# Optimization experiments

Hardware: AMD Instinct MI355X
Metric: run time of the kernel (lower is better)

The kernel has to match this reference:

```python
import jax, jax.numpy as jnp
import numpy as np

D_MODEL, D_INNER, D_STATE, D_CONV, DT_RANK = 512, 1024, 64, 4, 32
B, L = 2, 1000
EPS = 1e-5


def _rmsnorm(x, w):
    return x * jax.lax.rsqrt(jnp.mean(x * x, axis=-1, keepdims=True) + EPS) * w


def _causal_dwconv(x, w, b):
    # x: (B, L, Di); w: (Di, K) depthwise causal conv, output length L
    xT = jnp.transpose(x, (0, 2, 1))  # (B, Di, L)
    y = jax.lax.conv_general_dilated(
        xT, w[:, None, :], window_strides=(1,), padding=[(D_CONV - 1, 0)],
        dimension_numbers=('NCH', 'OIH', 'NCH'), feature_group_count=D_INNER)
    return jnp.transpose(y + b[None, :, None], (0, 2, 1))


def _selective_scan(u, dt, A, Bm, Cm):
    # u, dt: (B, L, Di); A: (Di, N); Bm, Cm: (B, L, N)
    def step(h, inp):
        dt_t, B_t, C_t, u_t = inp
        dA = jnp.exp(dt_t[..., None] * A)                       # (B, Di, N)
        h = dA * h + (dt_t * u_t)[..., None] * B_t[:, None, :]  # state update
        y = jnp.einsum('bdn,bn->bd', h, C_t)
        return h, y
    xs = (jnp.swapaxes(dt, 0, 1), jnp.swapaxes(Bm, 0, 1),
          jnp.swapaxes(Cm, 0, 1), jnp.swapaxes(u, 0, 1))
    h0 = jnp.zeros((u.shape[0], D_INNER, D_STATE), u.dtype)
    _, ys = jax.lax.scan(step, h0, xs)
    return jnp.swapaxes(ys, 0, 1)  # (B, L, Di)


def _mamba_layer(x, norm_w, in_proj, conv_w, conv_b, x_proj, dt_w, dt_b, A_log, Dp, out_proj):
    # mamba-ssm Block with fused_add_norm=False, n_layer=1:
    # residual = x; h = mixer(rmsnorm(x)); block output pair merges to h + x
    h = _rmsnorm(x, norm_w)
    xz = jnp.einsum('bld,ed->ble', h, in_proj)        # (B, L, 2*Di)
    xc, z = jnp.split(xz, 2, axis=-1)
    xc = jax.nn.silu(_causal_dwconv(xc, conv_w, conv_b))
    x_dbl = jnp.einsum('bld,ed->ble', xc, x_proj)     # (B, L, dt_rank + 2N)
    dt, Bm, Cm = jnp.split(x_dbl, [DT_RANK, DT_RANK + D_STATE], axis=-1)
    dt = jax.nn.softplus(jnp.einsum('blr,dr->bld', dt, dt_w) + dt_b)
    A = -jnp.exp(A_log)
    y = _selective_scan(xc, dt, A, Bm, Cm)
    y = (y + xc * Dp) * jax.nn.silu(z)
    return jnp.einsum('bld,ed->ble', y, out_proj) + x


def _forward(x,
             f_norm_w, f_in_proj, f_conv_w, f_conv_b, f_x_proj, f_dt_w, f_dt_b, f_A_log, f_D, f_out_proj,
             b_norm_w, b_in_proj, b_conv_w, b_conv_b, b_x_proj, b_dt_w, b_dt_b, b_A_log, b_D, b_out_proj):
    res_f = _mamba_layer(x, f_norm_w, f_in_proj, f_conv_w, f_conv_b, f_x_proj,
                         f_dt_w, f_dt_b, f_A_log, f_D, f_out_proj)
    res_b = _mamba_layer(jnp.flip(x, 1), b_norm_w, b_in_proj, b_conv_w, b_conv_b,
                         b_x_proj, b_dt_w, b_dt_b, b_A_log, b_D, b_out_proj)
    return res_f + jnp.flip(res_b, 1)  # bidirectional_merging='add'


def setup_inputs() -> dict:
    key = jax.random.key(0)
    ks = iter(jax.random.split(key, 32))
    def nrm(shape, s=0.02):
        return jax.random.normal(next(ks), shape, jnp.float32) * s
    inp = {'x': jax.random.normal(next(ks), (B, L, D_MODEL), jnp.float32)}
    for p in ('f', 'b'):
        inp[p + '_norm_w'] = jnp.ones((D_MODEL,), jnp.float32)
        inp[p + '_in_proj'] = nrm((2 * D_INNER, D_MODEL))
        inp[p + '_conv_w'] = nrm((D_INNER, D_CONV), 0.1)
        inp[p + '_conv_b'] = nrm((D_INNER,), 0.1)
        inp[p + '_x_proj'] = nrm((DT_RANK + 2 * D_STATE, D_INNER))
        inp[p + '_dt_w'] = nrm((D_INNER, DT_RANK), 0.1)
        inp[p + '_dt_b'] = jnp.full((D_INNER,), float(np.log(np.expm1(0.01))), jnp.float32)
        inp[p + '_A_log'] = jnp.log(jnp.tile(jnp.arange(1, D_STATE + 1, dtype=jnp.float32), (D_INNER, 1)))
        inp[p + '_D'] = jnp.ones((D_INNER,), jnp.float32)
        inp[p + '_out_proj'] = nrm((D_MODEL, D_INNER))
    return inp


def reference(x,
              f_norm_w, f_in_proj, f_conv_w, f_conv_b, f_x_proj, f_dt_w, f_dt_b, f_A_log, f_D, f_out_proj,
              b_norm_w, b_in_proj, b_conv_w, b_conv_b, b_x_proj, b_dt_w, b_dt_b, b_A_log, b_D, b_out_proj):
    return _forward(x,
                    f_norm_w, f_in_proj, f_conv_w, f_conv_b, f_x_proj, f_dt_w, f_dt_b, f_A_log, f_D, f_out_proj,
                    b_norm_w, b_in_proj, b_conv_w, b_conv_b, b_x_proj, b_dt_w, b_dt_b, b_A_log, b_D, b_out_proj)
```

## Files before the change

### kernel.cpp

```cpp
#include <hip/hip_runtime.h>
#include <hip/hip_bf16.h>
#include <math.h>

#define DM   512
#define DI   1024
#define NS   64
#define RDT  32
#define BB   2
#define LL   1000
#define MROWS (BB*LL)

typedef __attribute__((ext_vector_type(8))) short bf16x8;
typedef __attribute__((ext_vector_type(4))) float f32x4;

__device__ __forceinline__ unsigned short f2bf(float f) {
    unsigned u = __builtin_bit_cast(unsigned, f);
    u = (u + 0x7FFF + ((u >> 16) & 1)) >> 16;
    return (unsigned short)u;
}

__device__ __forceinline__ float bcast_lane(float v, int lane) {
    return __builtin_bit_cast(float,
        __builtin_amdgcn_readlane(__builtin_bit_cast(int, v), lane));
}

__global__ __launch_bounds__(256)
void rmsnorm_k(const float* __restrict__ x,
               const float* __restrict__ nw0, const float* __restrict__ nw1,
               unsigned short* __restrict__ xnb0, unsigned short* __restrict__ xnb1) {
    int row = blockIdx.x;
    int tid = threadIdx.x;
    const float* xr = x + (size_t)row * DM;
    float2 v = *(const float2*)(xr + tid * 2);
    float ss = v.x * v.x + v.y * v.y;
    #pragma unroll
    for (int off = 32; off; off >>= 1) ss += __shfl_xor(ss, off, 64);
    __shared__ float red[4];
    if ((tid & 63) == 0) red[tid >> 6] = ss;
    __syncthreads();
    float tot = red[0] + red[1] + red[2] + red[3];
    float scale = rsqrtf(tot / (float)DM + 1e-5f);
    float2 w0 = *(const float2*)(nw0 + tid * 2);
    float2 w1 = *(const float2*)(nw1 + tid * 2);
    short2 o0, o1;
    o0.x = (short)f2bf(v.x * scale * w0.x);
    o0.y = (short)f2bf(v.y * scale * w0.y);
    o1.x = (short)f2bf(v.x * scale * w1.x);
    o1.y = (short)f2bf(v.y * scale * w1.y);
    *(short2*)(xnb0 + (size_t)row * DM + tid * 2) = o0;
    *(short2*)(xnb1 + (size_t)row * DM + tid * 2) = o1;
}

__global__ __launch_bounds__(256)
void cvt2_k(const float* __restrict__ in0, const float* __restrict__ in1,
            unsigned short* __restrict__ out0, unsigned short* __restrict__ out1,
            int n4) {
    int idx = blockIdx.x * 256 + threadIdx.x;
    if (idx >= n4) return;
    const float* in = blockIdx.y ? in1 : in0;
    unsigned short* out = blockIdx.y ? out1 : out0;
    float4 v = *(const float4*)(in + (size_t)idx * 4);
    short4 o;
    o.x = (short)f2bf(v.x); o.y = (short)f2bf(v.y);
    o.z = (short)f2bf(v.z); o.w = (short)f2bf(v.w);
    *(short4*)(out + (size_t)idx * 4) = o;
}

__global__ __launch_bounds__(256, 2)
void gemm1_mfma(const unsigned short* __restrict__ xnb0,
                const unsigned short* __restrict__ xnb1,
                const unsigned short* __restrict__ wib0,
                const unsigned short* __restrict__ wib1,
                float* __restrict__ xz0, float* __restrict__ xz1)
{
    __shared__ __align__(16) unsigned short As[128 * 40];
    __shared__ __align__(16) unsigned short Bs[128 * 40];
    int dir = blockIdx.z;
    const unsigned short* A = dir ? xnb1 : xnb0;
    const unsigned short* W = dir ? wib1 : wib0;
    float* C = dir ? xz1 : xz0;
    int n0 = blockIdx.x * 128, m0 = blockIdx.y * 128;
    int tid = threadIdx.x;
    int wv = tid >> 6, lane = tid & 63;
    int wr = wv >> 1, wc = wv & 1;
    int fl = lane & 15, kg = lane >> 4;

    f32x4 acc[4][4];
    #pragma unroll
    for (int i = 0; i < 4; i++)
        #pragma unroll
        for (int j = 0; j < 4; j++) acc[i][j] = (f32x4){0.f, 0.f, 0.f, 0.f};

    int sr = tid >> 2, cg = tid & 3;
    for (int k0 = 0; k0 < 512; k0 += 32) {
        #pragma unroll
        for (int i = 0; i < 2; i++) {
            int row = sr + i * 64;
            int m = m0 + row;
            float4 av = make_float4(0.f, 0.f, 0.f, 0.f);
            if (m < MROWS) {
                int rs = m;
                if (dir) { int b = m / LL, t = m % LL; rs = b * LL + (LL - 1 - t); }
                av = *(const float4*)(A + (size_t)rs * 512 + k0 + cg * 8);
            }
            *(float4*)(&As[row * 40 + cg * 8]) = av;
            float4 wv4 = *(const float4*)(W + (size_t)(n0 + row) * 512 + k0 + cg * 8);
            *(float4*)(&Bs[row * 40 + cg * 8]) = wv4;
        }
        __syncthreads();
        bf16x8 af[4], bf[4];
        #pragma unroll
        for (int fr = 0; fr < 4; fr++)
            af[fr] = *(const bf16x8*)(&As[(wr * 64 + fr * 16 + fl) * 40 + kg * 8]);
        #pragma unroll
        for (int fc = 0; fc < 4; fc++)
            bf[fc] = *(const bf16x8*)(&Bs[(wc * 64 + fc * 16 + fl) * 40 + kg * 8]);
        #pragma unroll
        for (int fr = 0; fr < 4; fr++)
            #pragma unroll
            for (int fc = 0; fc < 4; fc++)
                acc[fr][fc] = __builtin_amdgcn_mfma_f32_16x16x32_bf16(
                    af[fr], bf[fc], acc[fr][fc], 0, 0, 0);
        __syncthreads();
    }
    #pragma unroll
    for (int fr = 0; fr < 4; fr++)
        #pragma unroll
        for (int fc = 0; fc < 4; fc++)
            #pragma unroll
            for (int j = 0; j < 4; j++) {
                int m = m0 + wr * 64 + fr * 16 + kg * 4 + j;
                if (m < MROWS) {
                    int n = n0 + wc * 64 + fc * 16 + fl;
                    C[(size_t)m * 2048 + n] = acc[fr][fc][j];
                }
            }
}

__global__ __launch_bounds__(256, 2)
void gemm_out_mfma(const unsigned short* __restrict__ ygb0,
                   const unsigned short* __restrict__ ygb1,
                   const unsigned short* __restrict__ wob0,
                   const unsigned short* __restrict__ wob1,
                   float* __restrict__ partial)
{
    __shared__ __align__(16) unsigned short As[64 * 40];
    __shared__ __align__(16) unsigned short Bs[64 * 40];
    int dir = blockIdx.z;
    const unsigned short* A = dir ? ygb1 : ygb0;
    const unsigned short* W = dir ? wob1 : wob0;
    float* P = partial + (size_t)dir * MROWS * 512;
    int n0 = blockIdx.x * 64, m0 = blockIdx.y * 64;
    int tid = threadIdx.x;
    int wv = tid >> 6, lane = tid & 63;
    int wr = wv >> 1, wc = wv & 1;
    int fl = lane & 15, kg = lane >> 4;

    f32x4 acc[2][2];
    #pragma unroll
    for (int i = 0; i < 2; i++)
        #pragma unroll
        for (int j = 0; j < 2; j++) acc[i][j] = (f32x4){0.f, 0.f, 0.f, 0.f};

    int sr = tid >> 2, cg = tid & 3;
    for (int k0 = 0; k0 < 1024; k0 += 32) {
        int m = m0 + sr;
        float4 av = make_float4(0.f, 0.f, 0.f, 0.f);
        if (m < MROWS)
            av = *(const float4*)(A + (size_t)m * 1024 + k0 + cg * 8);
        *(float4*)(&As[sr * 40 + cg * 8]) = av;
        float4 wv4 = *(const float4*)(W + (size_t)(n0 + sr) * 1024 + k0 + cg * 8);
        *(float4*)(&Bs[sr * 40 + cg * 8]) = wv4;
        __syncthreads();
        bf16x8 af[2], bf[2];
        #pragma unroll
        for (int fr = 0; fr < 2; fr++)
            af[fr] = *(const bf16x8*)(&As[(wr * 32 + fr * 16 + fl) * 40 + kg * 8]);
        #pragma unroll
        for (int fc = 0; fc < 2; fc++)
            bf[fc] = *(const bf16x8*)(&Bs[(wc * 32 + fc * 16 + fl) * 40 + kg * 8]);
        #pragma unroll
        for (int fr = 0; fr < 2; fr++)
            #pragma unroll
            for (int fc = 0; fc < 2; fc++)
                acc[fr][fc] = __builtin_amdgcn_mfma_f32_16x16x32_bf16(
                    af[fr], bf[fc], acc[fr][fc], 0, 0, 0);
        __syncthreads();
    }
    #pragma unroll
    for (int fr = 0; fr < 2; fr++)
        #pragma unroll
        for (int fc = 0; fc < 2; fc++)
            #pragma unroll
            for (int j = 0; j < 4; j++) {
                int m = m0 + wr * 32 + fr * 16 + kg * 4 + j;
                if (m < MROWS) {
                    int n = n0 + wc * 32 + fc * 16 + fl;
                    P[(size_t)m * 512 + n] = acc[fr][fc][j];
                }
            }
}

__global__ __launch_bounds__(256)
void reduce_out_k(const float* __restrict__ x, const float* __restrict__ partial,
                  float* __restrict__ out)
{
    int idx = blockIdx.x * 256 + threadIdx.x;
    if (idx >= MROWS * 128) return;
    int m = idx >> 7, q = idx & 127;
    int b = m / LL, t = m % LL;
    int fm = b * LL + (LL - 1 - t);
    const float* p0 = partial;
    const float* p1 = partial + (size_t)MROWS * 512;
    float4 xv = *(const float4*)(x  + (size_t)m  * 512 + q * 4);
    float4 a  = *(const float4*)(p0 + (size_t)m  * 512 + q * 4);
    float4 c  = *(const float4*)(p1 + (size_t)fm * 512 + q * 4);
    float4 o;
    o.x = 2.f * xv.x + a.x + c.x;
    o.y = 2.f * xv.y + a.y + c.y;
    o.z = 2.f * xv.z + a.z + c.z;
    o.w = 2.f * xv.w + a.w + c.w;
    *(float4*)(out + (size_t)m * 512 + q * 4) = o;
}

__global__ __launch_bounds__(256)
void conv_silu_k(const float* __restrict__ xz0, const float* __restrict__ xz1,
                 const float* __restrict__ cw0, const float* __restrict__ cw1,
                 const float* __restrict__ cb0, const float* __restrict__ cb1,
                 float* __restrict__ xcT0, float* __restrict__ xcT1)
{
    __shared__ float Ls[64 * 65];
    int dirb = blockIdx.z;
    int dir = dirb >> 1, b = dirb & 1;
    int d0 = blockIdx.x * 64, t0 = blockIdx.y * 64;
    int tid = threadIdx.x;
    int dl = tid & 63, tg = tid >> 6;

    const float* in = (dir ? xz1 : xz0) + (size_t)b * LL * 2048;
    const float* cw = dir ? cw1 : cw0;
    const float* cb = dir ? cb1 : cb0;
    float*      xcT = dir ? xcT1 : xcT0;

    float4 w4 = ((const float4*)cw)[d0 + dl];
    float bias = cb[d0 + dl];

    int ts = t0 + tg * 16;
    float x3 = 0.f, x2 = 0.f, x1 = 0.f;
    if (ts - 3 >= 0 && ts - 3 < LL) x3 = in[(size_t)(ts - 3) * 2048 + d0 + dl];
    if (ts - 2 >= 0 && ts - 2 < LL) x2 = in[(size_t)(ts - 2) * 2048 + d0 + dl];
    if (ts - 1 >= 0 && ts - 1 < LL) x1 = in[(size_t)(ts - 1) * 2048 + d0 + dl];

    #pragma unroll
    for (int i = 0; i < 16; i++) {
        int t = ts + i;
        float x0v = (t < LL) ? in[(size_t)t * 2048 + d0 + dl] : 0.f;
        float a = bias + x3 * w4.x + x2 * w4.y + x1 * w4.z + x0v * w4.w;
        float s = a / (1.f + __expf(-a));
        Ls[dl * 65 + tg * 16 + i] = s;
        x3 = x2; x2 = x1; x1 = x0v;
    }
    __syncthreads();
    int tl = tid & 63, dg = tid >> 6;
    #pragma unroll
    for (int i = 0; i < 16; i++) {
        int dd = dg * 16 + i;
        int t = t0 + tl;
        if (t < LL)
            xcT[((size_t)(b * 1024) + d0 + dd) * LL + t] = Ls[dd * 65 + tl];
    }
}

__global__ __launch_bounds__(256)
void gemm_xp_k(const float* __restrict__ xcT0, const float* __restrict__ xcT1,
               const float* __restrict__ xp0, const float* __restrict__ xp1,
               float* __restrict__ xd0, float* __restrict__ xd1,
               float* __restrict__ bct)
{
    __shared__ float As[16 * 68];
    __shared__ float Ws[16 * 68];
    __shared__ float T[64 * 67];
    int dirb = blockIdx.z;
    int dir = dirb >> 1, b = dirb & 1;
    const float* xcT = (dir ? xcT1 : xcT0) + (size_t)b * 1024 * LL;
    const float* W   = dir ? xp1 : xp0;
    float*       C   = (dir ? xd1 : xd0) + (size_t)b * LL * 160;
    int n0 = blockIdx.x * 64, t0 = blockIdx.y * 64;
    int tid = threadIdx.x;
    int tx = tid & 15, ty = tid >> 4;

    float acc[4][4] = {};

    for (int k0 = 0; k0 < 1024; k0 += 16) {
        {
            int kk = tid & 15, mq = tid >> 4;
            float4 v = make_float4(0.f, 0.f, 0.f, 0.f);
            if (t0 + mq * 4 + 3 < LL)
                v = *(const float4*)(xcT + (size_t)(k0 + kk) * LL + t0 + mq * 4);
            *(float4*)(As + kk * 68 + mq * 4) = v;
        }
        {
            int row = tid >> 2, q = tid & 3;
            float4 v = make_float4(0.f, 0.f, 0.f, 0.f);
            if (n0 + row < 160)
                v = *(const float4*)(W + (size_t)(n0 + row) * 1024 + k0 + q * 4);
            Ws[(q * 4 + 0) * 68 + row] = v.x;
            Ws[(q * 4 + 1) * 68 + row] = v.y;
            Ws[(q * 4 + 2) * 68 + row] = v.z;
            Ws[(q * 4 + 3) * 68 + row] = v.w;
        }
        __syncthreads();
        #pragma unroll
        for (int k = 0; k < 16; k++) {
            float4 a = *(const float4*)(As + k * 68 + ty * 4);
            float4 w = *(const float4*)(Ws + k * 68 + tx * 4);
            float av[4] = {a.x, a.y, a.z, a.w};
            float wvv[4] = {w.x, w.y, w.z, w.w};
            #pragma unroll
            for (int i = 0; i < 4; i++)
                #pragma unroll
                for (int j = 0; j < 4; j++)
                    acc[i][j] = fmaf(av[i], wvv[j], acc[i][j]);
        }
        __syncthreads();
    }

    if (n0 == 0) {
        #pragma unroll
        for (int i = 0; i < 4; i++) {
            int t = t0 + ty * 4 + i;
            if (t >= LL) continue;
            #pragma unroll
            for (int j = 0; j < 4; j++) {
                int n = tx * 4 + j;
                C[(size_t)t * 160 + n] = acc[i][j];
            }
        }
    }

    #pragma unroll
    for (int i = 0; i < 4; i++)
        #pragma unroll
        for (int j = 0; j < 4; j++)
            T[(tx * 4 + j) * 67 + ty * 4 + i] = acc[i][j];
    __syncthreads();
    int tl = tid & 63, ng = tid >> 6;
    #pragma unroll
    for (int i = 0; i < 16; i++) {
        int nl = ng * 16 + i;
        int n = n0 + nl;
        int t = t0 + tl;
        if (n >= 32 && n < 160 && t < LL)
            bct[((size_t)dirb * 128 + (n - 32)) * LL + t] = T[nl * 67 + tl];
    }
}

__global__ __launch_bounds__(256)
void gemm_dt_k(const float* __restrict__ xd0, const float* __restrict__ xd1,
               const float* __restrict__ w0, const float* __restrict__ w1,
               const float* __restrict__ bb0, const float* __restrict__ bb1,
               float* __restrict__ dtT0, float* __restrict__ dtT1)
{
    __shared__ float As[64 * 33];
    __shared__ float Ws[32 * 68];
    __shared__ float T[64 * 67];
    int dirb = blockIdx.z;
    int dir = dirb >> 1, b = dirb & 1;
    const float* xd = (dir ? xd1 : xd0) + (size_t)b * LL * 160;
    const float* W  = dir ? w1 : w0;
    const float* bi = dir ? bb1 : bb0;
    float*      dtT = (dir ? dtT1 : dtT0) + (size_t)b * 1024 * LL;
    int n0 = blockIdx.x * 64, t0 = blockIdx.y * 64;
    int tid = threadIdx.x;
    int tx = tid & 15, ty = tid >> 4;

    #pragma unroll
    for (int i = 0; i < 2; i++) {
        int j = tid + 256 * i;
        int row = j >> 3, q = j & 7;
        float4 v = make_float4(0.f, 0.f, 0.f, 0.f);
        if (t0 + row < LL)
            v = *(const float4*)(xd + (size_t)(t0 + row) * 160 + q * 4);
        As[row * 33 + q * 4 + 0] = v.x;
        As[row * 33 + q * 4 + 1] = v.y;
        As[row * 33 + q * 4 + 2] = v.z;
        As[row * 33 + q * 4 + 3] = v.w;
        float4 wv = *(const float4*)(W + (size_t)(n0 + row) * 32 + q * 4);
        Ws[(q * 4 + 0) * 68 + row] = wv.x;
        Ws[(q * 4 + 1) * 68 + row] = wv.y;
        Ws[(q * 4 + 2) * 68 + row] = wv.z;
        Ws[(q * 4 + 3) * 68 + row] = wv.w;
    }
    __syncthreads();

    float acc[4][4] = {};
    #pragma unroll 8
    for (int k = 0; k < 32; k++) {
        float4 w = *(const float4*)(Ws + k * 68 + tx * 4);
        float wvv[4] = {w.x, w.y, w.z, w.w};
        float av[4];
        #pragma unroll
        for (int i = 0; i < 4; i++) av[i] = As[(ty * 4 + i) * 33 + k];
        #pragma unroll
        for (int i = 0; i < 4; i++)
            #pragma unroll
            for (int j = 0; j < 4; j++)
                acc[i][j] = fmaf(av[i], wvv[j], acc[i][j]);
    }
    __syncthreads();

    #pragma unroll
    for (int i = 0; i < 4; i++) {
        #pragma unroll
        for (int j = 0; j < 4; j++) {
            int n = tx * 4 + j;
            float v = acc[i][j] + bi[n0 + n];
            v = (v > 20.f) ? v : log1pf(__expf(v));
            T[n * 67 + ty * 4 + i] = v;
        }
    }
    __syncthreads();

    int tl = tid & 63, ng = tid >> 6;
    #pragma unroll
    for (int i = 0; i < 16; i++) {
        int nl = ng * 16 + i;
        int t = t0 + tl;
        if (t < LL)
            dtT[(size_t)(n0 + nl) * LL + t] = T[nl * 67 + tl];
    }
}

__global__ __launch_bounds__(256)
void scan_k(float* __restrict__ dtT0, float* __restrict__ dtT1,
            const float* __restrict__ ucT0, const float* __restrict__ ucT1,
            const float* __restrict__ bct,
            const float* __restrict__ Al0, const float* __restrict__ Al1,
            const float* __restrict__ Dc0, const float* __restrict__ Dc1)
{
    __shared__ float Bs[64 * 34];
    __shared__ float Cs[64 * 34];
    __shared__ float Pt[4][16 * 66];
    int dirb = blockIdx.y;
    int dir = dirb >> 1, b = dirb & 1;
    int wid = threadIdx.x >> 6, lane = threadIdx.x & 63;
    int d = blockIdx.x * 4 + wid;
    float* Pw = Pt[wid];

    float*       dtT = (dir ? dtT1 : dtT0);
    const float* ucT = (dir ? ucT1 : ucT0);
    const float* Al  = dir ? Al1 : Al0;
    const float* Dc  = dir ? Dc1 : Dc0;

    float a    = -__expf(Al[d * 64 + lane]) * 1.44269504f;
    float Dp64 = Dc[d] * (1.f / 64.f);
    float h    = 0.f;
    size_t chan = ((size_t)(b * 1024 + d)) * LL;
    const float* Bg = bct + (size_t)dirb * 128 * LL;

    int srow = threadIdx.x >> 2;
    int scol = (threadIdx.x & 3) * 8;
    int tl16 = lane & 15, qq = lane >> 4;
    const float* Prow = Pw + tl16 * 66 + qq * 16;

    for (int t0 = 0; t0 < LL; t0 += 32) {
        int rem = min(32, LL - t0);
        __syncthreads();
        {
            float4 b0 = *(const float4*)(Bg + (size_t)srow * LL + t0 + scol);
            float4 b1 = *(const float4*)(Bg + (size_t)srow * LL + t0 + scol + 4);
            float4 c0 = *(const float4*)(Bg + (size_t)(srow + 64) * LL + t0 + scol);
            float4 c1 = *(const float4*)(Bg + (size_t)(srow + 64) * LL + t0 + scol + 4);
            *(float4*)(&Bs[srow * 34 + scol])     = b0;
            *(float4*)(&Bs[srow * 34 + scol + 4]) = b1;
            *(float4*)(&Cs[srow * 34 + scol])     = c0;
            *(float4*)(&Cs[srow * 34 + scol + 4]) = c1;
        }
        float dta = 0.f, ua = 0.f;
        if (lane < rem) {
            dta = dtT[chan + t0 + lane];
            ua  = ucT[chan + t0 + lane];
        }
        __syncthreads();

        for (int sec = 0; sec < 2; sec++) {
            int sbase = sec * 16;
            int steps = rem - sbase;
            if (steps <= 0) break;
            if (steps > 16) steps = 16;
            if (steps < 16) {
                for (int i = steps; i < 16; i++) Pw[i * 66 + lane] = 0.f;
            }
            int ngr = (steps + 7) >> 3;
            for (int g = 0; g < ngr; g++) {
                int tb = sbase + g * 8;
                float4 B0 = *(const float4*)(&Bs[lane * 34 + tb]);
                float4 B1 = *(const float4*)(&Bs[lane * 34 + tb + 4]);
                float4 C0 = *(const float4*)(&Cs[lane * 34 + tb]);
                float4 C1 = *(const float4*)(&Cs[lane * 34 + tb + 4]);
                #pragma unroll
                for (int i = 0; i < 8; i++) {
                    float dtv = bcast_lane(dta, tb + i);
                    float u   = bcast_lane(ua,  tb + i);
                    float dA  = exp2f(dtv * a);
                    float Bn  = (i < 4) ? B0[i] : B1[i - 4];
                    float Cn  = (i < 4) ? C0[i] : C1[i - 4];
                    h = fmaf(dA, h, dtv * u * Bn);
                    Pw[(g * 8 + i) * 66 + lane] = fmaf(u, Dp64, h * Cn);
                }
            }
            float s = 0.f;
            #pragma unroll
            for (int j = 0; j < 8; j++) {
                float2 v = *(const float2*)(Prow + j * 2);
                s += v.x + v.y;
            }
#if __has_builtin(__builtin_amdgcn_permlane32_swap)
            {
                unsigned aa = __builtin_bit_cast(unsigned, s);
                auto r = __builtin_amdgcn_permlane32_swap(aa, aa, false, false);
                s = __builtin_bit_cast(float, (unsigned)r[0]) +
                    __builtin_bit_cast(float, (unsigned)r[1]);
            }
#else
            s += __shfl_xor(s, 32, 64);
#endif
#if __has_builtin(__builtin_amdgcn_permlane16_swap)
            {
                unsigned aa = __builtin_bit_cast(unsigned, s);
                auto r = __builtin_amdgcn_permlane16_swap(aa, aa, false, false);
                s = __builtin_bit_cast(float, (unsigned)r[0]) +
                    __builtin_bit_cast(float, (unsigned)r[1]);
            }
#else
            s += __shfl_xor(s, 16, 64);
#endif
            if (lane < steps)
                dtT[chan + t0 + sbase + lane] = s;
        }
    }
}

__global__ __launch_bounds__(256)
void gate_k(const float* __restrict__ yT0, const float* __restrict__ yT1,
            const float* __restrict__ xz0, const float* __restrict__ xz1,
            unsigned short* __restrict__ yg0, unsigned short* __restrict__ yg1)
{
    __shared__ float Ls[64 * 65];
    int dirb = blockIdx.z;
    int dir = dirb >> 1, b = dirb & 1;
    int d0 = blockIdx.x * 64, t0 = blockIdx.y * 64;
    int tid = threadIdx.x;
    const float* yT = (dir ? yT1 : yT0) + (size_t)b * 1024 * LL;
    const float* xz = (dir ? xz1 : xz0) + (size_t)b * LL * 2048;
    unsigned short* yg = dir ? yg1 : yg0;

    int tl = tid & 63, dg = tid >> 6;
    #pragma unroll
    for (int i = 0; i < 16; i++) {
        int dd = dg * 16 + i;
        int t = t0 + tl;
        float v = (t < LL) ? yT[(size_t)(d0 + dd) * LL + t] : 0.f;
        Ls[dd * 65 + tl] = v;
    }
    __syncthreads();
    int dcol = tid & 63, tg = tid >> 6;
    #pragma unroll
    for (int i = 0; i < 16; i++) {
        int t = t0 + tg * 16 + i;
        if (t >= LL) continue;
        float z = xz[(size_t)t * 2048 + 1024 + d0 + dcol];
        float y = Ls[dcol * 65 + tg * 16 + i];
        float s = z / (1.f + __expf(-z));
        yg[((size_t)(b * LL + t)) * 1024 + d0 + dcol] = f2bf(y * s);
    }
}

extern "C" void kernel_launch(void* const* d_in, const int* in_sizes, int n_in,
                              void* d_out, int out_size, void* d_ws, size_t ws_size,
                              hipStream_t stream) {
    const float* x = (const float*)d_in[0];
    const float* P[2][10];
    for (int dir = 0; dir < 2; dir++)
        for (int i = 0; i < 10; i++)
            P[dir][i] = (const float*)d_in[1 + dir * 10 + i];

    float* ws = (float*)d_ws;
    float* xz0   = ws;
    float* xz1   = ws + 4096000;
    float* xcT0  = ws + 8192000;
    float* xcT1  = ws + 10240000;
    float* dtT0  = ws + 12288000;
    float* dtT1  = ws + 14336000;
    float* xdbl0 = ws + 16384000;
    float* xdbl1 = ws + 16704000;
    unsigned short* xnb0 = (unsigned short*)(ws + 17024000);
    unsigned short* xnb1 = (unsigned short*)(ws + 17280000);
    unsigned short* wib0 = (unsigned short*)dtT0;
    unsigned short* wib1 = (unsigned short*)dtT1;
    unsigned short* ygb0 = (unsigned short*)xcT0;
    unsigned short* ygb1 = (unsigned short*)xcT1;
    unsigned short* wob0 = (unsigned short*)dtT0;
    unsigned short* wob1 = (unsigned short*)dtT1;
    float* partial = xz0;
    float* bct = (float*)d_out;
    float* out = (float*)d_out;

    rmsnorm_k<<<MROWS, 256, 0, stream>>>(x, P[0][0], P[1][0], xnb0, xnb1);

    cvt2_k<<<dim3(1024, 2), 256, 0, stream>>>(P[0][1], P[1][1], wib0, wib1, 262144);

    gemm1_mfma<<<dim3(16, 16, 2), 256, 0, stream>>>(
        xnb0, xnb1, wib0, wib1, xz0, xz1);

    conv_silu_k<<<dim3(16, 16, 4), 256, 0, stream>>>(
        xz0, xz1, P[0][2], P[1][2], P[0][3], P[1][3], xcT0, xcT1);

    gemm_xp_k<<<dim3(3, 16, 4), 256, 0, stream>>>(
        xcT0, xcT1, P[0][4], P[1][4], xdbl0, xdbl1, bct);

    gemm_dt_k<<<dim3(16, 16, 4), 256, 0, stream>>>(
        xdbl0, xdbl1, P[0][5], P[1][5], P[0][6], P[1][6], dtT0, dtT1);

    scan_k<<<dim3(256, 4), 256, 0, stream>>>(
        dtT0, dtT1, xcT0, xcT1, bct,
        P[0][7], P[1][7], P[0][8], P[1][8]);

    gate_k<<<dim3(16, 16, 4), 256, 0, stream>>>(
        dtT0, dtT1, xz0, xz1, ygb0, ygb1);

    cvt2_k<<<dim3(512, 2), 256, 0, stream>>>(P[0][9], P[1][9], wob0, wob1, 131072);

    gemm_out_mfma<<<dim3(8, 32, 2), 256, 0, stream>>>(
        ygb0, ygb1, wob0, wob1, partial);

    reduce_out_k<<<1000, 256, 0, stream>>>(x, partial, out);
}
```

Baseline: 335.1 us.

## Prefetch next scan chunk into registers and simplify inner-loop arithmetic

The scan kernel now loads the next 32-step chunk of B/C and dt/u from global memory into registers while the current chunk is processed, so the loads overlap compute and one barrier wait on global latency is removed. The inner loop broadcasts a precomputed dt*u product instead of u, and the D-skip term moves out of the per-state partial sums to a single fma after the reduction. This costs extra registers and a shuffle per section, and floating-point summation order changes slightly.

```diff
diff --git a/kernel.cpp b/kernel.cpp
--- a/kernel.cpp
+++ b/kernel.cpp
@@ -451,9 +451,9 @@
     const float* Al  = dir ? Al1 : Al0;
     const float* Dc  = dir ? Dc1 : Dc0;
 
-    float a    = -__expf(Al[d * 64 + lane]) * 1.44269504f;
-    float Dp64 = Dc[d] * (1.f / 64.f);
-    float h    = 0.f;
+    float a  = -__expf(Al[d * 64 + lane]) * 1.44269504f;
+    float Dp = Dc[d];
+    float h  = 0.f;
     size_t chan = ((size_t)(b * 1024 + d)) * LL;
     const float* Bg = bct + (size_t)dirb * 128 * LL;
 
@@ -462,25 +462,40 @@
     int tl16 = lane & 15, qq = lane >> 4;
     const float* Prow = Pw + tl16 * 66 + qq * 16;
 
+    float4 rb0, rb1, rc0, rc1;
+    float dta = 0.f, ua = 0.f;
+    {
+        const float* Bp = Bg + (size_t)srow * LL + scol;
+        const float* Cp = Bg + (size_t)(srow + 64) * LL + scol;
+        rb0 = *(const float4*)(Bp);     rb1 = *(const float4*)(Bp + 4);
+        rc0 = *(const float4*)(Cp);     rc1 = *(const float4*)(Cp + 4);
+        if (lane < 32) {
+            dta = dtT[chan + lane];
+            ua  = ucT[chan + lane];
+        }
+    }
+
     for (int t0 = 0; t0 < LL; t0 += 32) {
         int rem = min(32, LL - t0);
         __syncthreads();
-        {
-            float4 b0 = *(const float4*)(Bg + (size_t)srow * LL + t0 + scol);
-            float4 b1 = *(const float4*)(Bg + (size_t)srow * LL + t0 + scol + 4);
-            float4 c0 = *(const float4*)(Bg + (size_t)(srow + 64) * LL + t0 + scol);
-            float4 c1 = *(const float4*)(Bg + (size_t)(srow + 64) * LL + t0 + scol + 4);
-            *(float4*)(&Bs[srow * 34 + scol])     = b0;
-            *(float4*)(&Bs[srow * 34 + scol + 4]) = b1;
-            *(float4*)(&Cs[srow * 34 + scol])     = c0;
-            *(float4*)(&Cs[srow * 34 + scol + 4]) = c1;
-        }
-        float dta = 0.f, ua = 0.f;
-        if (lane < rem) {
-            dta = dtT[chan + t0 + lane];
-            ua  = ucT[chan + t0 + lane];
-        }
-        __syncthreads();
+        *(float4*)(&Bs[srow * 34 + scol])     = rb0;
+        *(float4*)(&Bs[srow * 34 + scol + 4]) = rb1;
+        *(float4*)(&Cs[srow * 34 + scol])     = rc0;
+        *(float4*)(&Cs[srow * 34 + scol + 4]) = rc1;
+        float dcur = dta, ucur = ua;
+        float wsc  = dcur * ucur;
+        __syncthreads();
+
+        if (t0 + 32 < LL) {
+            const float* Bp = Bg + (size_t)srow * LL + (t0 + 32) + scol;
+            const float* Cp = Bg + (size_t)(srow + 64) * LL + (t0 + 32) + scol;
+            rb0 = *(const float4*)(Bp);     rb1 = *(const float4*)(Bp + 4);
+            rc0 = *(const float4*)(Cp);     rc1 = *(const float4*)(Cp + 4);
+            if (lane < min(32, LL - t0 - 32)) {
+                dta = dtT[chan + t0 + 32 + lane];
+                ua  = ucT[chan + t0 + 32 + lane];
+            }
+        }
 
         for (int sec = 0; sec < 2; sec++) {
             int sbase = sec * 16;
@@ -499,13 +514,13 @@
                 float4 C1 = *(const float4*)(&Cs[lane * 34 + tb + 4]);
                 #pragma unroll
                 for (int i = 0; i < 8; i++) {
-                    float dtv = bcast_lane(dta, tb + i);
-                    float u   = bcast_lane(ua,  tb + i);
+                    float dtv = bcast_lane(dcur, tb + i);
+                    float w   = bcast_lane(wsc,  tb + i);
                     float dA  = exp2f(dtv * a);
                     float Bn  = (i < 4) ? B0[i] : B1[i - 4];
                     float Cn  = (i < 4) ? C0[i] : C1[i - 4];
-                    h = fmaf(dA, h, dtv * u * Bn);
-                    Pw[(g * 8 + i) * 66 + lane] = fmaf(u, Dp64, h * Cn);
+                    h = fmaf(dA, h, w * Bn);
+                    Pw[(g * 8 + i) * 66 + lane] = h * Cn;
                 }
             }
             float s = 0.f;
@@ -534,6 +549,8 @@
 #else
             s += __shfl_xor(s, 16, 64);
 #endif
+            float uf = __shfl(ucur, sbase + tl16, 64);
+            s = fmaf(uf, Dp, s);
             if (lane < steps)
                 dtT[chan + t0 + sbase + lane] = s;
         }
```

New measurement: 316.0 us. -5.7%, faster.
